# Optimization experiments

Measured on AMD Instinct MI355X. Metric: run time of the kernel, lower is better.

Reference implementation:

```python
import jax, jax.numpy as jnp
import numpy as np

B, L, D, H = 8, 1024, 1024, 16
DH = D // H  # 64


def setup_inputs() -> dict:
    key = jax.random.key(0)
    ks = jax.random.split(key, 6)
    x = jax.random.normal(ks[0], (B, L, D), dtype=jnp.float32)
    mask = jax.random.randint(ks[1], (1, L, L), 0, 2).astype(jnp.float32)
    # params initialized ~ normal(std=0.1) as in the module's _initialize
    Wk = jax.random.normal(ks[2], (D, D), dtype=jnp.float32) * 0.1
    Wv = jax.random.normal(ks[3], (D, D), dtype=jnp.float32) * 0.1
    Wq = jax.random.normal(ks[4], (D, D), dtype=jnp.float32) * 0.1
    Wo = jax.random.normal(ks[5], (D, D), dtype=jnp.float32) * 0.1
    return {"x": x, "mask": mask, "Wk": Wk, "Wv": Wv, "Wq": Wq, "Wo": Wo}


def reference(x, mask, Wk, Wv, Wq, Wo):
    # torch Linear: y = x @ W.T
    k = jnp.einsum('bld,ed->ble', x, Wk).reshape(B, L, H, DH)
    v = jnp.einsum('bld,ed->ble', x, Wv).reshape(B, L, H, DH)
    q = jnp.einsum('bld,ed->ble', x, Wq).reshape(B, L, H, DH)
    # explicit score matrix [B, H, L, L]
    scores = jnp.einsum('blhe,bmhe->bhlm', q, k)
    m = mask[:, None]  # (1, 1, L, L) broadcasts over batch and heads
    scores = scores * m - 1e9 * (1.0 - m)
    scale = np.float32(1.0 / np.sqrt(DH))
    weights = jax.nn.softmax(scores * scale, axis=-1)
    out = jnp.einsum('bhlm,bmhe->blhe', weights, v).reshape(B, L, D)
    out = jnp.einsum('bld,ed->ble', out, Wo)  # output_linear (n_heads > 1)
    return out
```

## Files before the change

### kernel.cpp

```cpp
#include <hip/hip_runtime.h>

#define B_  8
#define L_  1024
#define D_  1024
#define H_  16
#define DH_ 64

typedef unsigned short u16;
typedef __attribute__((ext_vector_type(8))) short short8;
typedef __attribute__((ext_vector_type(8))) _Float16 half8;
typedef __attribute__((ext_vector_type(4))) float floatx4;
typedef __attribute__((ext_vector_type(16))) float floatx16;

static __device__ __forceinline__ u16 f2bf(float f) {
  union { float f; unsigned u; } cv; cv.f = f;
  unsigned u = cv.u;
  return (u16)((u + 0x7fffu + ((u >> 16) & 1u)) >> 16);
}
static __device__ __forceinline__ u16 f2h(float f) {
  union { _Float16 h; u16 u; } cv; cv.h = (_Float16)f; return cv.u;
}
static __device__ __forceinline__ unsigned pack_bf2(float a, float b) {
  union { float f; unsigned u; } ua, ub; ua.f = a; ub.f = b;
  return __builtin_amdgcn_perm(ub.u + 0x8000u, ua.u + 0x8000u, 0x07060302u);
}

__global__ void cast_all(const float* __restrict__ x,  const float* __restrict__ wq,
                         const float* __restrict__ wk, const float* __restrict__ wv,
                         const float* __restrict__ wo,
                         u16* __restrict__ xf,  u16* __restrict__ wqf,
                         u16* __restrict__ wkf, u16* __restrict__ wvf,
                         u16* __restrict__ wof) {
  int blk = blockIdx.x;
  const float* src; u16* dst; int off;
  if (blk < 8192)       { src = x;  dst = xf;  off = blk; }
  else if (blk < 9216)  { src = wq; dst = wqf; off = blk - 8192; }
  else if (blk < 10240) { src = wk; dst = wkf; off = blk - 9216; }
  else if (blk < 11264) { src = wv; dst = wvf; off = blk - 10240; }
  else                  { src = wo; dst = wof; off = blk - 11264; }
  int i = off * 1024 + threadIdx.x * 4;
  float4 f = *(const float4*)(src + i);
  ushort4 r;
  r.x = f2h(f.x); r.y = f2h(f.y); r.z = f2h(f.z); r.w = f2h(f.w);
  *(ushort4*)(dst + i) = r;
}

__global__ void bias_perm_kernel(const float* __restrict__ mask, float* __restrict__ biasP) {
  int i = blockIdx.x * 256 + threadIdx.x;
  int e = i & 3, lane = (i >> 2) & 63, rr = (i >> 8) & 3, t = (i >> 10) & 1;
  int c = (i >> 11) & 15, w = (i >> 15) & 3, qt = i >> 17;
  int reg = rr * 4 + e;
  int row = qt * 128 + w * 32 + (reg & 3) + 8 * (reg >> 2) + 4 * (lane >> 5);
  int key = c * 64 + t * 32 + (lane & 31);
  biasP[i] = (mask[(size_t)row * L_ + key] - 1.0f) * 1.25e8f - 24.0f;
}

typedef __attribute__((address_space(3))) void  lds_void;
typedef const __attribute__((address_space(1))) void g_void;
static __device__ __forceinline__ void load_lds16(const void* g, void* l) {
  __builtin_amdgcn_global_load_lds((g_void*)g, (lds_void*)l, 16, 0, 0);
}

__global__ __launch_bounds__(256) void gemm_qkv(const u16* __restrict__ A,
                                                const u16* __restrict__ wq,
                                                const u16* __restrict__ wk,
                                                const u16* __restrict__ wv,
                                                u16* __restrict__ qf,
                                                u16* __restrict__ kf,
                                                u16* __restrict__ vb) {
  const int K = D_, N = D_;
  int nb = blockIdx.x;
  const u16* Bw; u16* Cp; float scale; int obf;
  if (nb < 8)       { Bw = wq; Cp = qf; scale = 0.125f; obf = 0; }
  else if (nb < 16) { Bw = wk; Cp = kf; scale = 1.0f;   obf = 0; }
  else              { Bw = wv; Cp = vb; scale = 1.0f;   obf = 1; }
  const int n0 = (nb & 7) * 128;

  __shared__ u16 lA[128 * 32];
  __shared__ u16 lB[128 * 32];
  const int tid  = threadIdx.x;
  const int w    = tid >> 6;
  const int lane = tid & 63;
  const int m    = lane & 15;
  const int kg   = lane >> 4;
  const int m0   = blockIdx.y * 128;
  const int wm   = (w >> 1) * 64;
  const int wn   = (w & 1) * 64;
  const int rowS = tid >> 2;
  const int part = tid & 3;

  floatx4 acc[4][4];
#pragma unroll
  for (int i = 0; i < 4; ++i)
#pragma unroll
    for (int j = 0; j < 4; ++j)
#pragma unroll
      for (int r = 0; r < 4; ++r) acc[i][j][r] = 0.0f;

  for (int k0 = 0; k0 < K; k0 += 32) {
    __syncthreads();
#pragma unroll
    for (int rnd = 0; rnd < 2; ++rnd) {
      const u16* ga = A  + (size_t)(m0 + rnd * 64 + rowS) * K + k0 + part * 8;
      const u16* gb = Bw + (size_t)(n0 + rnd * 64 + rowS) * K + k0 + part * 8;
      load_lds16(ga, lA + rnd * 2048 + w * 512);
      load_lds16(gb, lB + rnd * 2048 + w * 512);
    }
    __syncthreads();

    half8 af[4], bf[4];
#pragma unroll
    for (int i = 0; i < 4; ++i) af[i] = *(const half8*)&lA[(wm + i * 16 + m) * 32 + kg * 8];
#pragma unroll
    for (int i = 0; i < 4; ++i) bf[i] = *(const half8*)&lB[(wn + i * 16 + m) * 32 + kg * 8];
#pragma unroll
    for (int mi = 0; mi < 4; ++mi)
#pragma unroll
      for (int ni = 0; ni < 4; ++ni)
        acc[mi][ni] = __builtin_amdgcn_mfma_f32_16x16x32_f16(af[mi], bf[ni], acc[mi][ni], 0, 0, 0);
  }

#pragma unroll
  for (int mi = 0; mi < 4; ++mi)
#pragma unroll
    for (int ni = 0; ni < 4; ++ni)
#pragma unroll
      for (int r = 0; r < 4; ++r) {
        int row = m0 + wm + mi * 16 + kg * 4 + r;
        int col = n0 + wn + ni * 16 + m;
        size_t idx = (size_t)row * N + col;
        float vv = acc[mi][ni][r] * scale;
        Cp[idx] = obf ? f2bf(vv) : f2h(vv);
      }
}

__global__ __launch_bounds__(256) void gemm_fin(const u16* __restrict__ A,
                                                const u16* __restrict__ Bw,
                                                float* __restrict__ Cp,
                                                int M, int N, int K) {
  __shared__ u16 lA[128 * 32];
  __shared__ u16 lB[128 * 32];
  const int tid  = threadIdx.x;
  const int w    = tid >> 6;
  const int lane = tid & 63;
  const int m    = lane & 15;
  const int kg   = lane >> 4;
  const int m0   = blockIdx.y * 128;
  const int n0   = blockIdx.x * 128;
  const int wm   = (w >> 1) * 64;
  const int wn   = (w & 1) * 64;
  const int rowS = tid >> 2;
  const int part = tid & 3;

  floatx4 acc[4][4];
#pragma unroll
  for (int i = 0; i < 4; ++i)
#pragma unroll
    for (int j = 0; j < 4; ++j)
#pragma unroll
      for (int r = 0; r < 4; ++r) acc[i][j][r] = 0.0f;

  for (int k0 = 0; k0 < K; k0 += 32) {
    __syncthreads();
#pragma unroll
    for (int rnd = 0; rnd < 2; ++rnd) {
      const u16* ga = A  + (size_t)(m0 + rnd * 64 + rowS) * K + k0 + part * 8;
      const u16* gb = Bw + (size_t)(n0 + rnd * 64 + rowS) * K + k0 + part * 8;
      load_lds16(ga, lA + rnd * 2048 + w * 512);
      load_lds16(gb, lB + rnd * 2048 + w * 512);
    }
    __syncthreads();

    half8 af[4], bf[4];
#pragma unroll
    for (int i = 0; i < 4; ++i) af[i] = *(const half8*)&lA[(wm + i * 16 + m) * 32 + kg * 8];
#pragma unroll
    for (int i = 0; i < 4; ++i) bf[i] = *(const half8*)&lB[(wn + i * 16 + m) * 32 + kg * 8];
#pragma unroll
    for (int mi = 0; mi < 4; ++mi)
#pragma unroll
      for (int ni = 0; ni < 4; ++ni)
        acc[mi][ni] = __builtin_amdgcn_mfma_f32_16x16x32_f16(af[mi], bf[ni], acc[mi][ni], 0, 0, 0);
  }

#pragma unroll
  for (int mi = 0; mi < 4; ++mi)
#pragma unroll
    for (int ni = 0; ni < 4; ++ni)
#pragma unroll
      for (int r = 0; r < 4; ++r) {
        int row = m0 + wm + mi * 16 + kg * 4 + r;
        int col = n0 + wn + ni * 16 + m;
        Cp[(size_t)row * N + col] = acc[mi][ni][r];
      }
}

__global__ __launch_bounds__(256) void transpose_v(const u16* __restrict__ v,
                                                   u16* __restrict__ vt) {
  __shared__ u16 lds[64][72];
  const int b  = blockIdx.y >> 4;
  const int h  = blockIdx.y & 15;
  const int l0 = blockIdx.x * 64;
  const int tid = threadIdx.x;
#pragma unroll
  for (int it = 0; it < 2; ++it) {
    int idx = it * 256 + tid;
    int i = idx >> 3, off = (idx & 7) * 8;
    *(short8*)&lds[i][off] =
        *(const short8*)(v + ((size_t)(b * L_ + l0 + i)) * D_ + h * 64 + off);
  }
  __syncthreads();
  const int j  = tid >> 2;
  const int p0 = (tid & 3) * 16;
  __attribute__((aligned(16))) u16 tmp[16];
#pragma unroll
  for (int s = 0; s < 16; ++s) {
    int p = p0 + s;
    int l = (p >> 1) + ((p & 1) << 5);
    tmp[s] = lds[l][j];
  }
  u16* dst = vt + ((size_t)((b * H_ + h) * DH_ + j)) * L_ + l0 + p0;
  *(short8*)(dst)     = *(const short8*)&tmp[0];
  *(short8*)(dst + 8) = *(const short8*)&tmp[8];
}

__global__ __launch_bounds__(256) void attn_kernel(const u16* __restrict__ q,
                                                   const u16* __restrict__ k,
                                                   const u16* __restrict__ vt,
                                                   const float* __restrict__ biasP,
                                                   u16* __restrict__ o) {
  __shared__ u16 lK[64][72];
  __shared__ u16 lVt[64][72];
  __shared__ u16 lP[4][32][72];

  const int bh = blockIdx.x, qt = blockIdx.y;
  const int b = bh >> 4, h = bh & 15;
  const int tid = threadIdx.x;
  const int w = tid >> 6, lane = tid & 63;
  const int c32 = lane & 31, hi = lane >> 5;
  const int qr0 = qt * 128 + w * 32;

  const int srow  = tid >> 3;
  const int skoff = (tid & 7) * 8;

  const size_t qbase = ((size_t)((b * L_ + qr0 + c32) * H_ + h)) * DH_;
  half8 aq[4];
#pragma unroll
  for (int ks = 0; ks < 4; ++ks)
    aq[ks] = *(const half8*)(q + qbase + ks * 16 + hi * 8);

  floatx16 acc0, acc1, sumacc;
#pragma unroll
  for (int i = 0; i < 16; ++i) { acc0[i] = 0.0f; acc1[i] = 0.0f; sumacc[i] = 0.0f; }

  short8 ones;
#pragma unroll
  for (int j = 0; j < 8; ++j) ones[j] = (short)0x3F80;

  short8 rk[2], rv[2];
#pragma unroll
  for (int it = 0; it < 2; ++it) {
    rk[it] = *(const short8*)(k + ((size_t)((b * L_ + it * 32 + srow) * H_ + h)) * DH_ + skoff);
    rv[it] = *(const short8*)(vt + ((size_t)((b * H_ + h) * DH_ + it * 32 + srow)) * L_ + skoff);
  }

  const float4* bias4 = (const float4*)(biasP + ((size_t)(qt * 4 + w) * 16) * 2048) + lane;

  for (int c = 0; c < 16; ++c) {
    __syncthreads();
#pragma unroll
    for (int it = 0; it < 2; ++it) {
      *(short8*)&lK[it * 32 + srow][skoff]  = rk[it];
      *(short8*)&lVt[it * 32 + srow][skoff] = rv[it];
    }
    __syncthreads();

    if (c < 15) {
      const int nb2 = (c + 1) * 64;
#pragma unroll
      for (int it = 0; it < 2; ++it) {
        rk[it] = *(const short8*)(k + ((size_t)((b * L_ + nb2 + it * 32 + srow) * H_ + h)) * DH_ + skoff);
        rv[it] = *(const short8*)(vt + ((size_t)((b * H_ + h) * DH_ + it * 32 + srow)) * L_ + nb2 + skoff);
      }
    }

    const float4* bp = bias4 + (size_t)c * 512;
    floatx16 s0, s1;
#pragma unroll
    for (int rr = 0; rr < 4; ++rr) {
      float4 b0 = bp[rr * 64];
      float4 b1 = bp[(4 + rr) * 64];
      s0[rr * 4 + 0] = b0.x; s0[rr * 4 + 1] = b0.y; s0[rr * 4 + 2] = b0.z; s0[rr * 4 + 3] = b0.w;
      s1[rr * 4 + 0] = b1.x; s1[rr * 4 + 1] = b1.y; s1[rr * 4 + 2] = b1.z; s1[rr * 4 + 3] = b1.w;
    }
#pragma unroll
    for (int ks = 0; ks < 4; ++ks) {
      half8 bk0 = *(const half8*)&lK[c32][ks * 16 + hi * 8];
      half8 bk1 = *(const half8*)&lK[32 + c32][ks * 16 + hi * 8];
      s0 = __builtin_amdgcn_mfma_f32_32x32x16_f16(aq[ks], bk0, s0, 0, 0, 0);
      s1 = __builtin_amdgcn_mfma_f32_32x32x16_f16(aq[ks], bk1, s1, 0, 0, 0);
    }

#pragma unroll
    for (int reg = 0; reg < 16; ++reg) {
      float p0 = __expf(s0[reg]);
      float p1 = __expf(s1[reg]);
      int row = (reg & 3) + 8 * (reg >> 2) + 4 * hi;
      *(unsigned*)&lP[w][row][c32 * 2] = pack_bf2(p0, p1);
    }

#pragma unroll
    for (int ks = 0; ks < 4; ++ks) {
      short8 ap  = *(const short8*)&lP[w][c32][ks * 16 + hi * 8];
      short8 bv0 = *(const short8*)&lVt[c32][ks * 16 + hi * 8];
      short8 bv1 = *(const short8*)&lVt[32 + c32][ks * 16 + hi * 8];
      acc0   = __builtin_amdgcn_mfma_f32_32x32x16_bf16(ap, bv0, acc0, 0, 0, 0);
      acc1   = __builtin_amdgcn_mfma_f32_32x32x16_bf16(ap, bv1, acc1, 0, 0, 0);
      sumacc = __builtin_amdgcn_mfma_f32_32x32x16_bf16(ap, ones, sumacc, 0, 0, 0);
    }
  }

#pragma unroll
  for (int reg = 0; reg < 16; ++reg) {
    int row = qr0 + (reg & 3) + 8 * (reg >> 2) + 4 * hi;
    float inv = 1.0f / sumacc[reg];
    size_t obase = ((size_t)((b * L_ + row) * H_ + h)) * DH_;
    o[obase + c32]      = f2h(acc0[reg] * inv);
    o[obase + 32 + c32] = f2h(acc1[reg] * inv);
  }
}

extern "C" void kernel_launch(void* const* d_in, const int* in_sizes, int n_in,
                              void* d_out, int out_size, void* d_ws, size_t ws_size,
                              hipStream_t stream) {
  const float* x    = (const float*)d_in[0];
  const float* mask = (const float*)d_in[1];
  const float* Wk   = (const float*)d_in[2];
  const float* Wv   = (const float*)d_in[3];
  const float* Wq   = (const float*)d_in[4];
  const float* Wo   = (const float*)d_in[5];

  char* ws = (char*)d_ws;
  u16* xf    = (u16*)(ws);
  u16* aout  = xf;
  u16* kf    = (u16*)(ws + (16ull << 20));
  u16* vtb   = (u16*)(ws + (32ull << 20));
  float* biasP = (float*)(ws + (48ull << 20));
  u16* wqf   = (u16*)(ws + (52ull << 20));
  u16* wkf   = (u16*)(ws + (54ull << 20));
  u16* wvf   = (u16*)(ws + (56ull << 20));
  u16* wof   = (u16*)(ws + (58ull << 20));
  u16* qf = (u16*)d_out;
  u16* vb = qf + (size_t)B_ * L_ * D_;

  cast_all<<<12288, 256, 0, stream>>>(x, Wq, Wk, Wv, Wo, xf, wqf, wkf, wvf, wof);
  bias_perm_kernel<<<4096, 256, 0, stream>>>(mask, biasP);

  gemm_qkv<<<dim3(24, 64), 256, 0, stream>>>(xf, wqf, wkf, wvf, qf, kf, vb);

  transpose_v<<<dim3(L_ / 64, B_ * H_), 256, 0, stream>>>(vb, vtb);

  attn_kernel<<<dim3(B_ * H_, L_ / 128), 256, 0, stream>>>(qf, kf, vtb, biasP, aout);

  gemm_fin<<<dim3(D_ / 128, (B_ * L_) / 128), 256, 0, stream>>>(
      aout, wof, (float*)d_out, B_ * L_, D_, D_);
}
```

Before: 284.9 us.

## Keep softmax probabilities in registers via transposed QK MFMA, prefetch bias, fuse bias kernel

Swaps the QK^T MFMA operands so the score tile comes out transposed, which puts each lane's exp values directly in the A-operand layout for the PV MFMA. This removes the per-wave LDS staging buffer for P and its write/read round trip. The bias permutation is changed to match the new layout, and its kernel is merged into the cast kernel to save a launch. The next chunk's bias is also prefetched into registers one iteration ahead. In exchange, register pressure rises from the eight float4 bias prefetch plus the packed P fragments.

```diff
diff --git a/kernel.cpp b/kernel.cpp
--- a/kernel.cpp
+++ b/kernel.cpp
@@ -27,11 +27,21 @@
 
 __global__ void cast_all(const float* __restrict__ x,  const float* __restrict__ wq,
                          const float* __restrict__ wk, const float* __restrict__ wv,
-                         const float* __restrict__ wo,
+                         const float* __restrict__ wo, const float* __restrict__ mask,
                          u16* __restrict__ xf,  u16* __restrict__ wqf,
                          u16* __restrict__ wkf, u16* __restrict__ wvf,
-                         u16* __restrict__ wof) {
+                         u16* __restrict__ wof, float* __restrict__ biasP) {
   int blk = blockIdx.x;
+  if (blk >= 12288) {
+    int i = (blk - 12288) * 256 + threadIdx.x;
+    int e = i & 3, lane = (i >> 2) & 63, rr = (i >> 8) & 3, t = (i >> 10) & 1;
+    int c = (i >> 11) & 15, w = (i >> 15) & 3, qt = i >> 17;
+    int kk  = e + 8 * rr + 4 * (lane >> 5);
+    int row = qt * 128 + w * 32 + (lane & 31);
+    int key = c * 64 + t * 32 + kk;
+    biasP[i] = (mask[(size_t)row * L_ + key] - 1.0f) * 1.25e8f - 24.0f;
+    return;
+  }
   const float* src; u16* dst; int off;
   if (blk < 8192)       { src = x;  dst = xf;  off = blk; }
   else if (blk < 9216)  { src = wq; dst = wqf; off = blk - 8192; }
@@ -43,16 +53,6 @@
   ushort4 r;
   r.x = f2h(f.x); r.y = f2h(f.y); r.z = f2h(f.z); r.w = f2h(f.w);
   *(ushort4*)(dst + i) = r;
-}
-
-__global__ void bias_perm_kernel(const float* __restrict__ mask, float* __restrict__ biasP) {
-  int i = blockIdx.x * 256 + threadIdx.x;
-  int e = i & 3, lane = (i >> 2) & 63, rr = (i >> 8) & 3, t = (i >> 10) & 1;
-  int c = (i >> 11) & 15, w = (i >> 15) & 3, qt = i >> 17;
-  int reg = rr * 4 + e;
-  int row = qt * 128 + w * 32 + (reg & 3) + 8 * (reg >> 2) + 4 * (lane >> 5);
-  int key = c * 64 + t * 32 + (lane & 31);
-  biasP[i] = (mask[(size_t)row * L_ + key] - 1.0f) * 1.25e8f - 24.0f;
 }
 
 typedef __attribute__((address_space(3))) void  lds_void;
@@ -231,7 +231,6 @@
                                                    u16* __restrict__ o) {
   __shared__ u16 lK[64][72];
   __shared__ u16 lVt[64][72];
-  __shared__ u16 lP[4][32][72];
 
   const int bh = blockIdx.x, qt = blockIdx.y;
   const int b = bh >> 4, h = bh & 15;
@@ -265,6 +264,9 @@
   }
 
   const float4* bias4 = (const float4*)(biasP + ((size_t)(qt * 4 + w) * 16) * 2048) + lane;
+  float4 bb[8];
+#pragma unroll
+  for (int r = 0; r < 8; ++r) bb[r] = bias4[r * 64];
 
   for (int c = 0; c < 16; ++c) {
     __syncthreads();
@@ -284,39 +286,43 @@
       }
     }
 
-    const float4* bp = bias4 + (size_t)c * 512;
     floatx16 s0, s1;
 #pragma unroll
     for (int rr = 0; rr < 4; ++rr) {
-      float4 b0 = bp[rr * 64];
-      float4 b1 = bp[(4 + rr) * 64];
+      float4 b0 = bb[rr];
+      float4 b1 = bb[rr + 4];
       s0[rr * 4 + 0] = b0.x; s0[rr * 4 + 1] = b0.y; s0[rr * 4 + 2] = b0.z; s0[rr * 4 + 3] = b0.w;
       s1[rr * 4 + 0] = b1.x; s1[rr * 4 + 1] = b1.y; s1[rr * 4 + 2] = b1.z; s1[rr * 4 + 3] = b1.w;
     }
+    if (c < 15) {
+      const float4* bp = bias4 + (size_t)(c + 1) * 512;
+#pragma unroll
+      for (int r = 0; r < 8; ++r) bb[r] = bp[r * 64];
+    }
+
 #pragma unroll
     for (int ks = 0; ks < 4; ++ks) {
       half8 bk0 = *(const half8*)&lK[c32][ks * 16 + hi * 8];
       half8 bk1 = *(const half8*)&lK[32 + c32][ks * 16 + hi * 8];
-      s0 = __builtin_amdgcn_mfma_f32_32x32x16_f16(aq[ks], bk0, s0, 0, 0, 0);
-      s1 = __builtin_amdgcn_mfma_f32_32x32x16_f16(aq[ks], bk1, s1, 0, 0, 0);
-    }
-
+      s0 = __builtin_amdgcn_mfma_f32_32x32x16_f16(bk0, aq[ks], s0, 0, 0, 0);
+      s1 = __builtin_amdgcn_mfma_f32_32x32x16_f16(bk1, aq[ks], s1, 0, 0, 0);
+    }
+
+    union { short8 v[4]; unsigned u[16]; } ap;
 #pragma unroll
     for (int reg = 0; reg < 16; ++reg) {
       float p0 = __expf(s0[reg]);
       float p1 = __expf(s1[reg]);
-      int row = (reg & 3) + 8 * (reg >> 2) + 4 * hi;
-      *(unsigned*)&lP[w][row][c32 * 2] = pack_bf2(p0, p1);
+      ap.u[reg] = pack_bf2(p0, p1);
     }
 
 #pragma unroll
     for (int ks = 0; ks < 4; ++ks) {
-      short8 ap  = *(const short8*)&lP[w][c32][ks * 16 + hi * 8];
       short8 bv0 = *(const short8*)&lVt[c32][ks * 16 + hi * 8];
       short8 bv1 = *(const short8*)&lVt[32 + c32][ks * 16 + hi * 8];
-      acc0   = __builtin_amdgcn_mfma_f32_32x32x16_bf16(ap, bv0, acc0, 0, 0, 0);
-      acc1   = __builtin_amdgcn_mfma_f32_32x32x16_bf16(ap, bv1, acc1, 0, 0, 0);
-      sumacc = __builtin_amdgcn_mfma_f32_32x32x16_bf16(ap, ones, sumacc, 0, 0, 0);
+      acc0   = __builtin_amdgcn_mfma_f32_32x32x16_bf16(ap.v[ks], bv0, acc0, 0, 0, 0);
+      acc1   = __builtin_amdgcn_mfma_f32_32x32x16_bf16(ap.v[ks], bv1, acc1, 0, 0, 0);
+      sumacc = __builtin_amdgcn_mfma_f32_32x32x16_bf16(ap.v[ks], ones, sumacc, 0, 0, 0);
     }
   }
 
@@ -353,8 +359,8 @@
   u16* qf = (u16*)d_out;
   u16* vb = qf + (size_t)B_ * L_ * D_;
 
-  cast_all<<<12288, 256, 0, stream>>>(x, Wq, Wk, Wv, Wo, xf, wqf, wkf, wvf, wof);
-  bias_perm_kernel<<<4096, 256, 0, stream>>>(mask, biasP);
+  cast_all<<<16384, 256, 0, stream>>>(x, Wq, Wk, Wv, Wo, mask,
+                                      xf, wqf, wkf, wvf, wof, biasP);
 
   gemm_qkv<<<dim3(24, 64), 256, 0, stream>>>(xf, wqf, wkf, wvf, qf, kf, vb);
 
```

After: 270.6 us. -5.0%, faster.
